# Kernel tuning notes

Measured on AMD Instinct MI355X. Metric: run time of the kernel, lower is better.

Reference implementation:

```python
import jax, jax.numpy as jnp
import numpy as np

N_CLASSES = 512


def setup_inputs() -> dict:
    key = jax.random.key(0)
    k1, k2 = jax.random.split(key)
    B, T, C, V = 16, 2048, 1, 256
    x0 = jax.random.normal(k1, (B, T, C, V), dtype=jnp.float32)
    # nn.Parameter(torch.randn(...) * embedding_scale) with embedding_scale = 0.001
    embedding0 = jax.random.normal(k2, (C, N_CLASSES, V), dtype=jnp.float32) * 0.001
    return {"x0": x0, "embedding0": embedding0}


def reference(x0, embedding0):
    # normalize=False path: x = x0, embedding = embedding0
    B, T, C, V = x0.shape
    K = embedding0.shape[1]
    x = x0
    emb = embedding0

    # Nearest-codebook search. Original materializes (chunk, C, K, V) diffs and
    # (same argmin) to avoid the huge broadcasted intermediate.
    x1 = x.reshape(B * T, C, V)                      # (N, C, V)
    x_sq = jnp.sum(x1 * x1, axis=-1)[:, :, None]     # (N, C, 1)
    e_sq = jnp.sum(emb * emb, axis=-1)[None]         # (1, C, K)
    cross = jnp.einsum('ncv,ckv->nck', x1, emb)      # (N, C, K)
    d2 = x_sq - 2.0 * cross + e_sq                   # (N, C, K)
    index = jnp.argmin(d2, axis=2)                   # (N, C) int

    # entropy of code usage (histogram over all selected indices)
    hist = jnp.bincount(index.reshape(-1), length=K).astype(jnp.float32)
    prob = hist / jnp.float32(index.shape[0])        # divide by N = len(index)
    entropy = -jnp.sum(jnp.where(hist > 0, prob * jnp.log(prob), 0.0))

    # gather codebook vectors
    offset = jnp.arange(C, dtype=index.dtype) * K    # (C,)
    index1 = (index + offset[None, :]).reshape(-1)   # (N*C,)
    output = emb.reshape(C * K, V)[index1].reshape(B, T, C, V)

    # straight-through output + VQ / commitment losses
    out0 = jax.lax.stop_gradient(output - x) + x
    out1 = jnp.sum((jax.lax.stop_gradient(x) - output) ** 2, axis=3)   # (B,T,C)
    out2 = jnp.sum((x - jax.lax.stop_gradient(output)) ** 2, axis=3) \
         + jnp.sum((x - x0) ** 2, axis=3)                              # zero term when normalize=False
    return out0, out1, out2, entropy
```

## Files before the change

### kernel.cpp

```cpp
#include <hip/hip_runtime.h>
#include <math.h>

#define NV 256
#define NK 512
#define TSH 4096
#define SLABR 128

typedef unsigned short u16;
typedef unsigned int u32;
using short8  = __attribute__((ext_vector_type(8))) short;
using floatx4 = __attribute__((ext_vector_type(4))) float;

__device__ __forceinline__ u16 f2bf(float f) {
    unsigned int u = __float_as_uint(f);
    u += 0x7fffu + ((u >> 16) & 1u);
    return (u16)(u >> 16);
}
__device__ __forceinline__ floatx4 mfma16(short8 a, short8 b, floatx4 c) {
    return __builtin_amdgcn_mfma_f32_16x16x32_bf16(a, b, c, 0, 0, 0);
}

__global__ __launch_bounds__(256) void vq_prepcvt(const float* __restrict__ emb,
                                                  float* __restrict__ esq1,
                                                  u16* __restrict__ ehws,
                                                  int* __restrict__ hist) {
    const int t = threadIdx.x;
    const int lane = t & 63;
    const int code = blockIdx.x * 4 + (t >> 6);
    const int nt = code >> 4, c = code & 15;
    const float4 v = *(const float4*)(emb + (size_t)code * NV + lane * 4);
    ushort4 h;
    h.x = f2bf(v.x);
    h.y = f2bf(v.y);
    h.z = f2bf(v.z);
    h.w = f2bf(v.w);
    const size_t base = (size_t)nt * TSH + (size_t)(lane >> 1) * 128 + c * 8 + (lane & 1) * 4;
    *(ushort4*)(ehws + base) = h;
    float s = v.x * v.x + v.y * v.y + v.z * v.z + v.w * v.w;
#pragma unroll
    for (int m = 1; m <= 32; m <<= 1) s += __shfl_xor(s, m, 64);
    if (lane == 0) esq1[code] = s + 2.0f;
    const int g = blockIdx.x * 256 + t;
    if (g < NK) hist[g] = 0;
}

__global__ __launch_bounds__(1024, 4) void vq_search(
    const float* __restrict__ x,
    const u16* __restrict__ ehws,
    const float* __restrict__ esq1,
    u32* __restrict__ idx_ws) {
    __shared__ u16 xl[2][16 * NV];
    __shared__ u32 kall[8][16][16];

    const int t = threadIdx.x;
    const int wid = t >> 6;
    const int lane = t & 63;
    const int lr = lane & 15;
    const int lg = lane >> 4;
    const size_t row0 = (size_t)blockIdx.x * SLABR;

    const u16* bb0 = ehws + (size_t)(2 * wid) * TSH + lane * 8;
    const u16* bb1 = ehws + (size_t)(2 * wid + 1) * TSH + lane * 8;
    short8 b0[8], b1[8];
#pragma unroll
    for (int ks = 0; ks < 8; ++ks) {
        b0[ks] = *(const short8*)(bb0 + ks * 512);
        b1[ks] = *(const short8*)(bb1 + ks * 512);
    }
    const float evq0 = esq1[(2 * wid) * 16 + lr];
    const float evq1 = esq1[(2 * wid + 1) * 16 + lr];
    const u32 cid0 = (u32)((2 * wid) * 16 + lr);
    const u32 cid1 = (u32)((2 * wid + 1) * 16 + lr);

#define XLOAD(XR, TAU)                                                         \
    XR = *(const float4*)(x + (row0 + (TAU) * 16 + wid) * NV + lane * 4)
#define XWRITE(XR, BUF) do {                                                   \
        u32 lo = (u32)f2bf(XR.x) | ((u32)f2bf(XR.y) << 16);                    \
        u32 hi = (u32)f2bf(XR.z) | ((u32)f2bf(XR.w) << 16);                    \
        int byte = wid * 512 + ((lane * 8) ^ ((wid & 7) << 4));                \
        *(uint2*)((char*)&xl[BUF][0] + byte) = make_uint2(lo, hi);             \
    } while (0)

    float4 xr;
    XLOAD(xr, 0);
    XWRITE(xr, 0);
    __syncthreads();

#pragma unroll 2
    for (int tau = 0; tau < 8; ++tau) {
        const int buf = tau & 1;
        if (tau < 7) XLOAD(xr, tau + 1);

        floatx4 a0e = {0.f,0.f,0.f,0.f}, a0o = {0.f,0.f,0.f,0.f};
        floatx4 a1e = {0.f,0.f,0.f,0.f}, a1o = {0.f,0.f,0.f,0.f};
#pragma unroll
        for (int ks = 0; ks < 8; ++ks) {
            int byte = lr * 512 + ((ks * 64 + lg * 16) ^ ((lr & 7) << 4));
            short8 a = *(const short8*)((const char*)&xl[buf][0] + byte);
            if (ks & 1) { a0o = mfma16(a, b0[ks], a0o); a1o = mfma16(a, b1[ks], a1o); }
            else        { a0e = mfma16(a, b0[ks], a0e); a1e = mfma16(a, b1[ks], a1e); }
        }
        u32 rmin[4];
#pragma unroll
        for (int j = 0; j < 4; ++j) {
            float d0 = fmaf(-2.0f, a0e[j] + a0o[j], evq0);
            float d1 = fmaf(-2.0f, a1e[j] + a1o[j], evq1);
            u32 k0 = (__float_as_uint(d0) & 0xfffffe00u) | cid0;
            u32 k1 = (__float_as_uint(d1) & 0xfffffe00u) | cid1;
            rmin[j] = min(k0, k1);
        }
#pragma unroll
        for (int j = 0; j < 4; ++j) {
#pragma unroll
            for (int m = 1; m <= 8; m <<= 1) {
                u32 v = (u32)__shfl_xor((int)rmin[j], m, 64);
                rmin[j] = min(rmin[j], v);
            }
        }
        if (lr == 0) {
#pragma unroll
            for (int j = 0; j < 4; ++j) kall[tau][wid][lg * 4 + j] = rmin[j];
        }

        if (tau < 7) XWRITE(xr, buf ^ 1);
        __syncthreads();
    }
#undef XLOAD
#undef XWRITE

    if (t < SLABR) {
        u32 v = 0xffffffffu;
#pragma unroll
        for (int w = 0; w < 16; ++w) v = min(v, kall[t >> 4][w][t & 15]);
        idx_ws[row0 + t] = v & 511u;
    }
}

__global__ __launch_bounds__(256) void vq_epi(
    const float* __restrict__ x,
    const float* __restrict__ emb,
    const u32* __restrict__ idx_ws,
    int* __restrict__ hist,
    float* __restrict__ out0,
    float* __restrict__ out1,
    float* __restrict__ out2) {
    const int t = threadIdx.x;
    const int wid = t >> 6;
    const int lane = t & 63;
    const size_t rbase = ((size_t)blockIdx.x * 4 + wid) * 8;

    int idx[8];
#pragma unroll
    for (int rr = 0; rr < 8; ++rr) idx[rr] = (int)idx_ws[rbase + rr];

    float s[8];
#pragma unroll
    for (int rr = 0; rr < 8; ++rr) {
        const size_t row = rbase + rr;
        const float4 xv = *(const float4*)(x + row * NV + lane * 4);
        const float4 ev = *(const float4*)(emb + (size_t)idx[rr] * NV + lane * 4);
        float4 o;
        o.x = (ev.x - xv.x) + xv.x;
        o.y = (ev.y - xv.y) + xv.y;
        o.z = (ev.z - xv.z) + xv.z;
        o.w = (ev.w - xv.w) + xv.w;
        *(float4*)(out0 + row * NV + lane * 4) = o;
        float d0 = xv.x - ev.x, d1 = xv.y - ev.y, d2 = xv.z - ev.z, d3 = xv.w - ev.w;
        s[rr] = d0 * d0 + d1 * d1 + d2 * d2 + d3 * d3;
    }
#pragma unroll
    for (int rr = 0; rr < 8; ++rr) {
#pragma unroll
        for (int m = 1; m <= 32; m <<= 1) s[rr] += __shfl_xor(s[rr], m, 64);
    }
    if (lane == 0) {
#pragma unroll
        for (int rr = 0; rr < 8; ++rr) {
            out1[rbase + rr] = s[rr];
            out2[rbase + rr] = s[rr];
            atomicAdd(&hist[idx[rr]], 1);
        }
    }
}

__global__ __launch_bounds__(256) void vq_entropy(const int* __restrict__ hist,
                                                  float* __restrict__ out_ent,
                                                  int n_rows) {
    __shared__ float sdata[256];
    int t = threadIdx.x;
    float local = 0.0f;
    float invn = 1.0f / (float)n_rows;
    for (int k = t; k < NK; k += 256) {
        int h = hist[k];
        if (h > 0) {
            float p = (float)h * invn;
            local += p * logf(p);
        }
    }
    sdata[t] = local;
    __syncthreads();
    for (int s = 128; s >= 1; s >>= 1) {
        if (t < s) sdata[t] += sdata[t + s];
        __syncthreads();
    }
    if (t == 0) *out_ent = -sdata[0];
}

extern "C" void kernel_launch(void* const* d_in, const int* in_sizes, int n_in,
                              void* d_out, int out_size, void* d_ws, size_t ws_size,
                              hipStream_t stream) {
    const float* x   = (const float*)d_in[0];
    const float* emb = (const float*)d_in[1];

    const int n_rows = in_sizes[0] / NV;

    float* out0 = (float*)d_out;
    float* out1 = out0 + (size_t)n_rows * NV;
    float* out2 = out1 + n_rows;
    float* ent  = out2 + n_rows;

    float* esq1  = (float*)d_ws;
    int* hist    = (int*)(esq1 + NK);
    u32* idx_ws  = (u32*)(hist + NK + 4);
    u16* ehws    = (u16*)(idx_ws + n_rows);

    vq_prepcvt<<<NK / 4, 256, 0, stream>>>(emb, esq1, ehws, hist);
    vq_search<<<n_rows / SLABR, 1024, 0, stream>>>(x, ehws, esq1, idx_ws);
    vq_epi<<<n_rows / 32, 256, 0, stream>>>(x, emb, idx_ws, hist,
                                            out0, out1, out2);
    vq_entropy<<<1, 256, 0, stream>>>(hist, ent, n_rows);
}
```

Measured before the change: 54.67 us.

## Fuse search and epilogue kernels into one, keeping indices in LDS

The separate epilogue kernel is merged into the search kernel. After each 128-row slab's argmin, the indices stay in shared memory and the same block gathers codebook rows, writes out0/out1/out2 and updates the histogram. This removes one kernel launch, the index workspace round trip, and a second pass that reloads x from a cold cache, since x rows are likely still in L2. In exchange the epilogue now runs at the search kernel's occupancy, and it cannot overlap with other blocks' search work the way a separate kernel's blocks could.

```diff
diff --git a/kernel.cpp b/kernel.cpp
--- a/kernel.cpp
+++ b/kernel.cpp
@@ -44,13 +44,18 @@
     if (g < NK) hist[g] = 0;
 }
 
-__global__ __launch_bounds__(1024, 4) void vq_search(
+__global__ __launch_bounds__(1024, 4) void vq_main(
     const float* __restrict__ x,
+    const float* __restrict__ emb,
     const u16* __restrict__ ehws,
     const float* __restrict__ esq1,
-    u32* __restrict__ idx_ws) {
+    int* __restrict__ hist,
+    float* __restrict__ out0,
+    float* __restrict__ out1,
+    float* __restrict__ out2) {
     __shared__ u16 xl[2][16 * NV];
     __shared__ u32 kall[8][16][16];
+    __shared__ u32 idx_lds[SLABR];
 
     const int t = threadIdx.x;
     const int wid = t >> 6;
@@ -132,53 +137,51 @@
         u32 v = 0xffffffffu;
 #pragma unroll
         for (int w = 0; w < 16; ++w) v = min(v, kall[t >> 4][w][t & 15]);
-        idx_ws[row0 + t] = v & 511u;
-    }
-}
-
-__global__ __launch_bounds__(256) void vq_epi(
-    const float* __restrict__ x,
-    const float* __restrict__ emb,
-    const u32* __restrict__ idx_ws,
-    int* __restrict__ hist,
-    float* __restrict__ out0,
-    float* __restrict__ out1,
-    float* __restrict__ out2) {
-    const int t = threadIdx.x;
-    const int wid = t >> 6;
-    const int lane = t & 63;
-    const size_t rbase = ((size_t)blockIdx.x * 4 + wid) * 8;
-
-    int idx[8];
-#pragma unroll
-    for (int rr = 0; rr < 8; ++rr) idx[rr] = (int)idx_ws[rbase + rr];
-
-    float s[8];
-#pragma unroll
-    for (int rr = 0; rr < 8; ++rr) {
-        const size_t row = rbase + rr;
-        const float4 xv = *(const float4*)(x + row * NV + lane * 4);
-        const float4 ev = *(const float4*)(emb + (size_t)idx[rr] * NV + lane * 4);
-        float4 o;
-        o.x = (ev.x - xv.x) + xv.x;
-        o.y = (ev.y - xv.y) + xv.y;
-        o.z = (ev.z - xv.z) + xv.z;
-        o.w = (ev.w - xv.w) + xv.w;
-        *(float4*)(out0 + row * NV + lane * 4) = o;
-        float d0 = xv.x - ev.x, d1 = xv.y - ev.y, d2 = xv.z - ev.z, d3 = xv.w - ev.w;
-        s[rr] = d0 * d0 + d1 * d1 + d2 * d2 + d3 * d3;
-    }
-#pragma unroll
-    for (int rr = 0; rr < 8; ++rr) {
-#pragma unroll
-        for (int m = 1; m <= 32; m <<= 1) s[rr] += __shfl_xor(s[rr], m, 64);
-    }
-    if (lane == 0) {
-#pragma unroll
-        for (int rr = 0; rr < 8; ++rr) {
-            out1[rbase + rr] = s[rr];
-            out2[rbase + rr] = s[rr];
-            atomicAdd(&hist[idx[rr]], 1);
+        const int idx = (int)(v & 511u);
+        idx_lds[t] = (u32)idx;
+        atomicAdd(&hist[idx], 1);
+    }
+    __syncthreads();
+
+    const size_t rb = row0 + (size_t)wid * 8;
+#pragma unroll
+    for (int batch = 0; batch < 2; ++batch) {
+        const int r0 = batch * 4;
+        int idx4[4];
+#pragma unroll
+        for (int rr = 0; rr < 4; ++rr) idx4[rr] = (int)idx_lds[wid * 8 + r0 + rr];
+        float4 xv[4], ev[4];
+#pragma unroll
+        for (int rr = 0; rr < 4; ++rr) {
+            const size_t row = rb + r0 + rr;
+            xv[rr] = *(const float4*)(x + row * NV + lane * 4);
+            ev[rr] = *(const float4*)(emb + (size_t)idx4[rr] * NV + lane * 4);
+        }
+        float s[4];
+#pragma unroll
+        for (int rr = 0; rr < 4; ++rr) {
+            const size_t row = rb + r0 + rr;
+            float4 o;
+            o.x = (ev[rr].x - xv[rr].x) + xv[rr].x;
+            o.y = (ev[rr].y - xv[rr].y) + xv[rr].y;
+            o.z = (ev[rr].z - xv[rr].z) + xv[rr].z;
+            o.w = (ev[rr].w - xv[rr].w) + xv[rr].w;
+            *(float4*)(out0 + row * NV + lane * 4) = o;
+            float d0 = xv[rr].x - ev[rr].x, d1 = xv[rr].y - ev[rr].y;
+            float d2 = xv[rr].z - ev[rr].z, d3 = xv[rr].w - ev[rr].w;
+            s[rr] = d0 * d0 + d1 * d1 + d2 * d2 + d3 * d3;
+        }
+#pragma unroll
+        for (int rr = 0; rr < 4; ++rr) {
+#pragma unroll
+            for (int m = 1; m <= 32; m <<= 1) s[rr] += __shfl_xor(s[rr], m, 64);
+        }
+        if (lane == 0) {
+#pragma unroll
+            for (int rr = 0; rr < 4; ++rr) {
+                out1[rb + r0 + rr] = s[rr];
+                out2[rb + r0 + rr] = s[rr];
+            }
         }
     }
 }
@@ -221,12 +224,10 @@
 
     float* esq1  = (float*)d_ws;
     int* hist    = (int*)(esq1 + NK);
-    u32* idx_ws  = (u32*)(hist + NK + 4);
-    u16* ehws    = (u16*)(idx_ws + n_rows);
+    u16* ehws    = (u16*)(hist + NK + 4);
 
     vq_prepcvt<<<NK / 4, 256, 0, stream>>>(emb, esq1, ehws, hist);
-    vq_search<<<n_rows / SLABR, 1024, 0, stream>>>(x, ehws, esq1, idx_ws);
-    vq_epi<<<n_rows / 32, 256, 0, stream>>>(x, emb, idx_ws, hist,
-                                            out0, out1, out2);
+    vq_main<<<n_rows / SLABR, 1024, 0, stream>>>(x, emb, ehws, esq1, hist,
+                                                 out0, out1, out2);
     vq_entropy<<<1, 256, 0, stream>>>(hist, ent, n_rows);
 }
```

After: 45.21 us. -17.3%, faster.
